# Performance work log

Hardware: AMD Instinct MI355X
Metric: run time of the kernel (lower is better)

Reference implementation:

```python
import jax, jax.numpy as jnp
import numpy as np

L, B, D, H = 2048, 2, 1024, 16
DK = D // H
SCALE = DK ** -0.5


def setup_inputs() -> dict:
    key = jax.random.key(0)
    ks = jax.random.split(key, 11)
    w_std = D ** -0.5
    return {
        "query": jax.random.normal(ks[0], (L, B, D), dtype=jnp.float32),
        "key": jax.random.normal(ks[1], (L, B, D), dtype=jnp.float32),
        "value": jax.random.normal(ks[2], (L, B, D), dtype=jnp.float32),
        "WQ_w": jax.random.normal(ks[3], (D, D), dtype=jnp.float32) * w_std,
        "WQ_b": jnp.zeros((D,), dtype=jnp.float32),
        "WK_w": jax.random.normal(ks[4], (D, D), dtype=jnp.float32) * w_std,
        "WK_b": jnp.zeros((D,), dtype=jnp.float32),
        "WV_w": jax.random.normal(ks[5], (D, D), dtype=jnp.float32) * w_std,
        "WV_b": jnp.zeros((D,), dtype=jnp.float32),
        "WO_w": jax.random.normal(ks[6], (D, D), dtype=jnp.float32) * w_std,
        "WO_b": jnp.zeros((D,), dtype=jnp.float32),
    }


def reference(query, key, value, WQ_w, WQ_b, WK_w, WK_b, WV_w, WV_b, WO_w, WO_b):
    tgt_len, batch, _ = query.shape
    src_len = key.shape[0]
    # linear projections (torch Linear: x @ W^T + b)
    q = (query @ WQ_w.T + WQ_b) * SCALE            # [L, B, D]
    k = key @ WK_w.T + WK_b                        # [S, B, D]
    v = value @ WV_w.T + WV_b                      # [S, B, D]
    # split heads: [len, B, D] -> [B*H, len, DK]
    q = q.reshape(tgt_len, batch * H, DK).transpose(1, 0, 2)
    k = k.reshape(src_len, batch * H, DK).transpose(1, 0, 2)
    v = v.reshape(src_len, batch * H, DK).transpose(1, 0, 2)
    # attention scores and softmax (full [B*H, L, S] matrix, as in the original)
    scores = jnp.einsum('nld,nsd->nls', q, k)      # [B*H, L, S]
    probs = jax.nn.softmax(scores, axis=-1)
    out = jnp.einsum('nls,nsd->nld', probs, v)     # [B*H, L, DK]
    # merge heads: [B*H, L, DK] -> [L, B, D]
    out = out.transpose(1, 0, 2).reshape(tgt_len, batch, D)
    return out @ WO_w.T + WO_b
```

## Files before the change

### kernel.cpp

```cpp
#include <hip/hip_runtime.h>
#include <hip/hip_fp16.h>

#define LL 2048
#define BB 2
#define DD 1024
#define HH 16
#define DKK 64

typedef _Float16 h8 __attribute__((ext_vector_type(8)));
typedef _Float16 h4 __attribute__((ext_vector_type(4)));
typedef float f4 __attribute__((ext_vector_type(4)));
typedef float f16v __attribute__((ext_vector_type(16)));

#define BAR() do {                                              \
    asm volatile("s_waitcnt lgkmcnt(0)" ::: "memory");          \
    __builtin_amdgcn_s_barrier();                               \
    asm volatile("" ::: "memory");                              \
} while (0)

__device__ __forceinline__ void gload_lds16(const void* g, void* l) {
    __builtin_amdgcn_global_load_lds(
        (const __attribute__((address_space(1))) void*)g,
        (__attribute__((address_space(3))) void*)l, 16, 0, 0);
}

__device__ __forceinline__ unsigned pack2h(float a, float b) {
    union { _Float16 h[2]; unsigned u; } x;
    x.h[0] = (_Float16)a; x.h[1] = (_Float16)b;
    return x.u;
}

__global__ __launch_bounds__(256) void cvt_all(
    const float* __restrict__ x0, const float* __restrict__ x1,
    const float* __restrict__ x2, const float* __restrict__ w0,
    const float* __restrict__ w1, const float* __restrict__ w2,
    const float* __restrict__ w3,
    _Float16* __restrict__ y0, _Float16* __restrict__ y1,
    _Float16* __restrict__ y2, _Float16* __restrict__ z0,
    _Float16* __restrict__ z1, _Float16* __restrict__ z2,
    _Float16* __restrict__ z3)
{
    const int sel = blockIdx.y;
    if (sel >= 3 && blockIdx.x >= 512) return;
    const float* src = (sel == 0) ? x0 : (sel == 1) ? x1 : (sel == 2) ? x2
                     : (sel == 3) ? w0 : (sel == 4) ? w1 : (sel == 5) ? w2 : w3;
    _Float16* dst = (sel == 0) ? y0 : (sel == 1) ? y1 : (sel == 2) ? y2
                  : (sel == 3) ? z0 : (sel == 4) ? z1 : (sel == 5) ? z2 : z3;
    const int i = (blockIdx.x * 256 + threadIdx.x) * 8;
    f4 a = *(const f4*)(src + i);
    f4 b = *(const f4*)(src + i + 4);
    h8 o = {(_Float16)a.x, (_Float16)a.y, (_Float16)a.z, (_Float16)a.w,
            (_Float16)b.x, (_Float16)b.y, (_Float16)b.z, (_Float16)b.w};
    *(h8*)(dst + i) = o;
}

__global__ __launch_bounds__(256) void qkv_proj(
    const _Float16* __restrict__ xq, const _Float16* __restrict__ xk,
    const _Float16* __restrict__ xv,
    const _Float16* __restrict__ wq, const float* __restrict__ bq,
    const _Float16* __restrict__ wk, const float* __restrict__ bk,
    const _Float16* __restrict__ wv, const float* __restrict__ bv,
    _Float16* __restrict__ qh, _Float16* __restrict__ kh,
    _Float16* __restrict__ vth)
{
    const int mode = blockIdx.z;
    const _Float16* X    = (mode == 0) ? xq : (mode == 1) ? xk : xv;
    const _Float16* W    = (mode == 0) ? wq : (mode == 1) ? wk : wv;
    const float*    bias = (mode == 0) ? bq : (mode == 1) ? bk : bv;

    __shared__ alignas(16) _Float16 a_sm[128 * 32];
    __shared__ alignas(16) _Float16 b_sm[128 * 32];

    const int tid  = threadIdx.x;
    const int lane = tid & 63;
    const int wave = tid >> 6;
    const int wm = (wave & 1) * 64;
    const int wn = (wave >> 1) * 64;
    const int m0 = blockIdx.x * 128;
    const int n0 = blockIdx.y * 128;

    const int srow = tid >> 2;
    const int scol = (tid & 3) * 8;
    const int lds_base = wave * 512;

    f4 acc[4][4];
    #pragma unroll
    for (int i = 0; i < 4; i++)
        #pragma unroll
        for (int j = 0; j < 4; j++)
            #pragma unroll
            for (int r = 0; r < 4; r++) acc[i][j][r] = 0.f;

    const int fr = lane & 15;
    const int fk = (lane >> 4) * 8;

    for (int k0 = 0; k0 < DD; k0 += 32) {
        gload_lds16(X + (size_t)(m0 + srow) * DD + k0 + scol,       &a_sm[lds_base]);
        gload_lds16(X + (size_t)(m0 + 64 + srow) * DD + k0 + scol,  &a_sm[2048 + lds_base]);
        gload_lds16(W + (size_t)(n0 + srow) * DD + k0 + scol,       &b_sm[lds_base]);
        gload_lds16(W + (size_t)(n0 + 64 + srow) * DD + k0 + scol,  &b_sm[2048 + lds_base]);
        __syncthreads();
        h8 af[4], bfr[4];
        #pragma unroll
        for (int i = 0; i < 4; i++) af[i]  = *(const h8*)&a_sm[(wm + i * 16 + fr) * 32 + fk];
        #pragma unroll
        for (int j = 0; j < 4; j++) bfr[j] = *(const h8*)&b_sm[(wn + j * 16 + fr) * 32 + fk];
        #pragma unroll
        for (int i = 0; i < 4; i++)
            #pragma unroll
            for (int j = 0; j < 4; j++)
                acc[i][j] = __builtin_amdgcn_mfma_f32_16x16x32_f16(af[i], bfr[j], acc[i][j], 0, 0, 0);
        __syncthreads();
    }

    const int colc = lane & 15;
    const int rowb = (lane >> 4) * 4;
    #pragma unroll
    for (int i = 0; i < 4; i++) {
        #pragma unroll
        for (int j = 0; j < 4; j++) {
            const int nn = n0 + wn + j * 16 + colc;
            const float bval = bias[nn];
            #pragma unroll
            for (int reg = 0; reg < 4; reg++) {
                const int mm = m0 + wm + i * 16 + rowb + reg;
                float v = acc[i][j][reg] + bval;
                const int b = mm & 1, l = mm >> 1;
                const int h = nn >> 6, dk = nn & 63;
                const int head = b * HH + h;
                if (mode == 0) {
                    v *= 0.1803368801111243f;
                    qh[((size_t)head * LL + l) * DKK + dk] = (_Float16)v;
                } else if (mode == 1) {
                    kh[((size_t)head * LL + l) * DKK + dk] = (_Float16)v;
                } else {
                    vth[((size_t)head * DKK + dk) * LL + l] = (_Float16)v;
                }
            }
        }
    }
}

__global__ __launch_bounds__(256, 2) void attn(
    const _Float16* __restrict__ qh, const _Float16* __restrict__ kh,
    const _Float16* __restrict__ vth, _Float16* __restrict__ oh)
{
    const int head = blockIdx.y;
    const int q0   = blockIdx.x * 128;
    const int tid = threadIdx.x, lane = tid & 63, wave = tid >> 6;
    const int qw = q0 + wave * 32;

    __shared__ alignas(16) _Float16 k_sm[128][72];
    __shared__ alignas(16) _Float16 vt_sm[64][136];
    __shared__ float ls_sm[4][32];

    const int rq = lane & 31;
    const int hi = lane >> 5;
    const int kb = hi * 8;
    const int tid8 = tid * 8;

    const _Float16* khead  = kh  + (size_t)head * LL * DKK;
    const _Float16* vthead = vth + (size_t)head * DKK * LL;

    const _Float16* qbase = qh + ((size_t)head * LL + qw + rq) * DKK;
    h8 qa[4];
    #pragma unroll
    for (int kf = 0; kf < 4; kf++) qa[kf] = *(const h8*)(qbase + kf * 16 + kb);

    f16v o0, o1;
    #pragma unroll
    for (int r = 0; r < 16; r++) { o0[r] = 0.f; o1[r] = 0.f; }
    float lsum = 0.f;

    #pragma unroll
    for (int t = 0; t < 4; t++) {
        const int flat = t * 2048 + tid8;
        *(h8*)&k_sm[flat >> 6][flat & 63] = *(const h8*)(khead + flat);
        *(h8*)&vt_sm[flat >> 7][flat & 127] =
            *(const h8*)(vthead + (size_t)(flat >> 7) * LL + (flat & 127));
    }
    BAR();

    for (int it = 0; it < 16; ++it) {
        const int s1 = it * 128 + 128;
        const bool more = (s1 < LL);

        h8 kpre[4], vpre[4];
        if (more) {
            const _Float16* kg = khead + (size_t)s1 * DKK;
            #pragma unroll
            for (int t = 0; t < 4; t++) kpre[t] = *(const h8*)(kg + t * 2048 + tid8);
            #pragma unroll
            for (int t = 0; t < 4; t++) {
                const int flat = t * 2048 + tid8;
                vpre[t] = *(const h8*)(vthead + (size_t)(flat >> 7) * LL + s1 + (flat & 127));
            }
        }

        f16v sc[4];
        #pragma unroll
        for (int st = 0; st < 4; st++) {
            #pragma unroll
            for (int r = 0; r < 16; r++) sc[st][r] = 0.f;
            #pragma unroll
            for (int kf = 0; kf < 4; kf++) {
                h8 kf8 = *(const h8*)&k_sm[st * 32 + rq][kf * 16 + kb];
                sc[st] = __builtin_amdgcn_mfma_f32_32x32x16_f16(kf8, qa[kf], sc[st], 0, 0, 0);
            }
        }

        #pragma unroll
        for (int st = 0; st < 4; st++) {
            float p[16];
            #pragma unroll
            for (int r = 0; r < 16; r++) {
                p[r] = __builtin_amdgcn_exp2f(sc[st][r]);
                lsum += p[r];
            }
            unsigned own[4][2], part[4][2];
            #pragma unroll
            for (int g = 0; g < 4; g++) {
                own[g][0] = pack2h(p[4 * g],     p[4 * g + 1]);
                own[g][1] = pack2h(p[4 * g + 2], p[4 * g + 3]);
                part[g][0] = __shfl_xor(own[g][0], 32, 64);
                part[g][1] = __shfl_xor(own[g][1], 32, 64);
            }
            #pragma unroll
            for (int j = 0; j < 2; j++) {
                union { unsigned u[4]; h8 h; } pa;
                pa.u[0] = hi ? part[2 * j + 1][0] : own[2 * j][0];
                pa.u[1] = hi ? part[2 * j + 1][1] : own[2 * j][1];
                pa.u[2] = hi ? own[2 * j + 1][0]  : part[2 * j][0];
                pa.u[3] = hi ? own[2 * j + 1][1]  : part[2 * j][1];
                h8 b0 = *(const h8*)&vt_sm[rq][st * 32 + j * 16 + kb];
                h8 b1 = *(const h8*)&vt_sm[32 + rq][st * 32 + j * 16 + kb];
                o0 = __builtin_amdgcn_mfma_f32_32x32x16_f16(pa.h, b0, o0, 0, 0, 0);
                o1 = __builtin_amdgcn_mfma_f32_32x32x16_f16(pa.h, b1, o1, 0, 0, 0);
            }
        }

        BAR();
        if (more) {
            #pragma unroll
            for (int t = 0; t < 4; t++) {
                const int flat = t * 2048 + tid8;
                *(h8*)&k_sm[flat >> 6][flat & 63] = kpre[t];
            }
            #pragma unroll
            for (int t = 0; t < 4; t++) {
                const int flat = t * 2048 + tid8;
                *(h8*)&vt_sm[flat >> 7][flat & 127] = vpre[t];
            }
            BAR();
        }
    }

    lsum += __shfl_xor(lsum, 32, 64);
    ls_sm[wave][rq] = 1.0f / lsum;
    asm volatile("s_waitcnt lgkmcnt(0)" ::: "memory");

    const int b = head >> 4, h = head & 15;
    #pragma unroll
    for (int r = 0; r < 16; r++) {
        const int qrow = (r & 3) + 8 * (r >> 2) + 4 * hi;
        const float inv = ls_sm[wave][qrow];
        const int ql = qw + qrow;
        const size_t base = (size_t)(ql * BB + b) * DD + h * DKK;
        oh[base + rq]      = (_Float16)(o0[r] * inv);
        oh[base + 32 + rq] = (_Float16)(o1[r] * inv);
    }
}

__global__ __launch_bounds__(256) void out_proj(
    const _Float16* __restrict__ oh, const _Float16* __restrict__ wo,
    const float* __restrict__ bo, float* __restrict__ out)
{
    __shared__ alignas(16) _Float16 a_sm[64 * 32];
    __shared__ alignas(16) _Float16 b_sm[128 * 32];
    const int tid = threadIdx.x, lane = tid & 63, wave = tid >> 6;
    const int wm = (wave & 1) * 32, wn = (wave >> 1) * 64;
    const int m0 = blockIdx.x * 64, n0 = blockIdx.y * 128;

    const int srow = tid >> 2;
    const int scol = (tid & 3) * 8;
    const int lds_base = wave * 512;

    f4 acc[2][4];
    #pragma unroll
    for (int i = 0; i < 2; i++)
        #pragma unroll
        for (int j = 0; j < 4; j++)
            #pragma unroll
            for (int r = 0; r < 4; r++) acc[i][j][r] = 0.f;

    const int fr = lane & 15;
    const int fk = (lane >> 4) * 8;

    for (int k0 = 0; k0 < DD; k0 += 32) {
        gload_lds16(oh + (size_t)(m0 + srow) * DD + k0 + scol,      &a_sm[lds_base]);
        gload_lds16(wo + (size_t)(n0 + srow) * DD + k0 + scol,      &b_sm[lds_base]);
        gload_lds16(wo + (size_t)(n0 + 64 + srow) * DD + k0 + scol, &b_sm[2048 + lds_base]);
        __syncthreads();
        h8 af[2], bfr[4];
        #pragma unroll
        for (int i = 0; i < 2; i++) af[i]  = *(const h8*)&a_sm[(wm + i * 16 + fr) * 32 + fk];
        #pragma unroll
        for (int j = 0; j < 4; j++) bfr[j] = *(const h8*)&b_sm[(wn + j * 16 + fr) * 32 + fk];
        #pragma unroll
        for (int i = 0; i < 2; i++)
            #pragma unroll
            for (int j = 0; j < 4; j++)
                acc[i][j] = __builtin_amdgcn_mfma_f32_16x16x32_f16(af[i], bfr[j], acc[i][j], 0, 0, 0);
        __syncthreads();
    }

    const int colc = lane & 15;
    const int rowb = (lane >> 4) * 4;
    #pragma unroll
    for (int i = 0; i < 2; i++) {
        #pragma unroll
        for (int j = 0; j < 4; j++) {
            const int nn = n0 + wn + j * 16 + colc;
            const float bval = bo[nn];
            #pragma unroll
            for (int reg = 0; reg < 4; reg++) {
                const int mm = m0 + wm + i * 16 + rowb + reg;
                out[(size_t)mm * DD + nn] = acc[i][j][reg] + bval;
            }
        }
    }
}

extern "C" void kernel_launch(void* const* d_in, const int* in_sizes, int n_in,
                              void* d_out, int out_size, void* d_ws, size_t ws_size,
                              hipStream_t stream) {
    const float* qin = (const float*)d_in[0];
    const float* kin = (const float*)d_in[1];
    const float* vin = (const float*)d_in[2];
    const float* wq  = (const float*)d_in[3];
    const float* bq  = (const float*)d_in[4];
    const float* wk  = (const float*)d_in[5];
    const float* bk  = (const float*)d_in[6];
    const float* wv  = (const float*)d_in[7];
    const float* bv  = (const float*)d_in[8];
    const float* wo  = (const float*)d_in[9];
    const float* bo  = (const float*)d_in[10];

    const size_t seg = (size_t)32 * LL * DKK;
    _Float16* qh  = (_Float16*)d_ws;
    _Float16* kh  = qh + seg;
    _Float16* vth = kh + seg;
    _Float16* oh  = vth + seg;
    _Float16* wqh = oh + seg;
    _Float16* wkh = wqh + (size_t)DD * DD;
    _Float16* wvh = wkh + (size_t)DD * DD;
    _Float16* woh = wvh + (size_t)DD * DD;
    _Float16* xqh = woh + (size_t)DD * DD;
    _Float16* xkh = xqh + seg;
    _Float16* xvh = xkh + seg;

    hipLaunchKernelGGL(cvt_all, dim3(2048, 7), dim3(256), 0, stream,
                       qin, kin, vin, wq, wk, wv, wo,
                       xqh, xkh, xvh, wqh, wkh, wvh, woh);
    hipLaunchKernelGGL(qkv_proj, dim3(32, 8, 3), dim3(256), 0, stream,
                       xqh, xkh, xvh, wqh, bq, wkh, bk, wvh, bv, qh, kh, vth);
    hipLaunchKernelGGL(attn, dim3(16, 32), dim3(256), 0, stream, qh, kh, vth, oh);
    hipLaunchKernelGGL(out_proj, dim3(64, 8), dim3(256), 0, stream, oh, woh,
                       bo, (float*)d_out);
}
```

Before: 225.7 us.

## Split key tiles across paired waves in attention and remap block order

The attention kernel now runs 512 threads per block. Two waves share each 32-row query strip, and each takes half of every 128-key tile. At the end, the partial outputs and row sums are combined through LDS, reusing the K/V tile region as the exchange buffer. Block indices are also remapped so that consecutive blocks are spread across heads and query tiles. The goal is more waves in flight per CU to hide MFMA and load latency, and better L2 locality. The costs are an extra LDS reduction and tighter register limits from __launch_bounds__(512,4), which could cause spills.

New measurement: 225.9 us. About the same (+0.1%).

```diff
diff --git a/kernel.cpp b/kernel.cpp
--- a/kernel.cpp
+++ b/kernel.cpp
@@ -141,18 +141,25 @@
     }
 }
 
-__global__ __launch_bounds__(256, 2) void attn(
+__global__ __launch_bounds__(512, 4) void attn(
     const _Float16* __restrict__ qh, const _Float16* __restrict__ kh,
     const _Float16* __restrict__ vth, _Float16* __restrict__ oh)
 {
-    const int head = blockIdx.y;
-    const int q0   = blockIdx.x * 128;
+    const int rb = blockIdx.y * 16 + blockIdx.x;
+    const int lb = (rb & 7) * 64 + (rb >> 3);
+    const int head = lb >> 4;
+    const int q0   = (lb & 15) * 128;
+
     const int tid = threadIdx.x, lane = tid & 63, wave = tid >> 6;
-    const int qw = q0 + wave * 32;
-
-    __shared__ alignas(16) _Float16 k_sm[128][72];
-    __shared__ alignas(16) _Float16 vt_sm[64][136];
-    __shared__ float ls_sm[4][32];
+    const int qstrip = wave & 3;
+    const int sh     = wave >> 2;
+    const int qw = q0 + qstrip * 32;
+
+    __shared__ alignas(16) char smem_raw[128 * 72 * 2 + 64 * 136 * 2 + 4 * 32 * 4];
+    _Float16 (*k_sm)[72]   = (_Float16(*)[72])smem_raw;
+    _Float16 (*vt_sm)[136] = (_Float16(*)[136])(smem_raw + 18432);
+    float    (*ls_sm)[32]  = (float(*)[32])(smem_raw + 18432 + 17408);
+    float*   xch           = (float*)smem_raw;
 
     const int rq = lane & 31;
     const int hi = lane >> 5;
@@ -173,8 +180,8 @@
     float lsum = 0.f;
 
     #pragma unroll
-    for (int t = 0; t < 4; t++) {
-        const int flat = t * 2048 + tid8;
+    for (int t = 0; t < 2; t++) {
+        const int flat = t * 4096 + tid8;
         *(h8*)&k_sm[flat >> 6][flat & 63] = *(const h8*)(khead + flat);
         *(h8*)&vt_sm[flat >> 7][flat & 127] =
             *(const h8*)(vthead + (size_t)(flat >> 7) * LL + (flat & 127));
@@ -185,36 +192,38 @@
         const int s1 = it * 128 + 128;
         const bool more = (s1 < LL);
 
-        h8 kpre[4], vpre[4];
+        h8 kpre[2], vpre[2];
         if (more) {
             const _Float16* kg = khead + (size_t)s1 * DKK;
             #pragma unroll
-            for (int t = 0; t < 4; t++) kpre[t] = *(const h8*)(kg + t * 2048 + tid8);
-            #pragma unroll
-            for (int t = 0; t < 4; t++) {
-                const int flat = t * 2048 + tid8;
+            for (int t = 0; t < 2; t++) kpre[t] = *(const h8*)(kg + t * 4096 + tid8);
+            #pragma unroll
+            for (int t = 0; t < 2; t++) {
+                const int flat = t * 4096 + tid8;
                 vpre[t] = *(const h8*)(vthead + (size_t)(flat >> 7) * LL + s1 + (flat & 127));
             }
         }
 
-        f16v sc[4];
-        #pragma unroll
-        for (int st = 0; st < 4; st++) {
-            #pragma unroll
-            for (int r = 0; r < 16; r++) sc[st][r] = 0.f;
+        f16v sc[2];
+        #pragma unroll
+        for (int st2 = 0; st2 < 2; st2++) {
+            const int st = sh * 2 + st2;
+            #pragma unroll
+            for (int r = 0; r < 16; r++) sc[st2][r] = 0.f;
             #pragma unroll
             for (int kf = 0; kf < 4; kf++) {
                 h8 kf8 = *(const h8*)&k_sm[st * 32 + rq][kf * 16 + kb];
-                sc[st] = __builtin_amdgcn_mfma_f32_32x32x16_f16(kf8, qa[kf], sc[st], 0, 0, 0);
-            }
-        }
-
-        #pragma unroll
-        for (int st = 0; st < 4; st++) {
+                sc[st2] = __builtin_amdgcn_mfma_f32_32x32x16_f16(kf8, qa[kf], sc[st2], 0, 0, 0);
+            }
+        }
+
+        #pragma unroll
+        for (int st2 = 0; st2 < 2; st2++) {
+            const int st = sh * 2 + st2;
             float p[16];
             #pragma unroll
             for (int r = 0; r < 16; r++) {
-                p[r] = __builtin_amdgcn_exp2f(sc[st][r]);
+                p[r] = __builtin_amdgcn_exp2f(sc[st2][r]);
                 lsum += p[r];
             }
             unsigned own[4][2], part[4][2];
@@ -242,13 +251,13 @@
         BAR();
         if (more) {
             #pragma unroll
-            for (int t = 0; t < 4; t++) {
-                const int flat = t * 2048 + tid8;
+            for (int t = 0; t < 2; t++) {
+                const int flat = t * 4096 + tid8;
                 *(h8*)&k_sm[flat >> 6][flat & 63] = kpre[t];
             }
             #pragma unroll
-            for (int t = 0; t < 4; t++) {
-                const int flat = t * 2048 + tid8;
+            for (int t = 0; t < 2; t++) {
+                const int flat = t * 4096 + tid8;
                 *(h8*)&vt_sm[flat >> 7][flat & 127] = vpre[t];
             }
             BAR();
@@ -256,18 +265,31 @@
     }
 
     lsum += __shfl_xor(lsum, 32, 64);
-    ls_sm[wave][rq] = 1.0f / lsum;
-    asm volatile("s_waitcnt lgkmcnt(0)" ::: "memory");
-
-    const int b = head >> 4, h = head & 15;
-    #pragma unroll
-    for (int r = 0; r < 16; r++) {
-        const int qrow = (r & 3) + 8 * (r >> 2) + 4 * hi;
-        const float inv = ls_sm[wave][qrow];
-        const int ql = qw + qrow;
-        const size_t base = (size_t)(ql * BB + b) * DD + h * DKK;
-        oh[base + rq]      = (_Float16)(o0[r] * inv);
-        oh[base + 32 + rq] = (_Float16)(o1[r] * inv);
+
+    float* myx = xch + ((qstrip * 64 + lane) * 33);
+    if (sh) {
+        #pragma unroll
+        for (int r = 0; r < 16; r++) { myx[r] = o0[r]; myx[16 + r] = o1[r]; }
+        myx[32] = lsum;
+    }
+    BAR();
+    if (!sh) {
+        #pragma unroll
+        for (int r = 0; r < 16; r++) { o0[r] += myx[r]; o1[r] += myx[16 + r]; }
+        lsum += myx[32];
+        ls_sm[wave][rq] = 1.0f / lsum;
+        asm volatile("s_waitcnt lgkmcnt(0)" ::: "memory");
+
+        const int b = head >> 4, h = head & 15;
+        #pragma unroll
+        for (int r = 0; r < 16; r++) {
+            const int qrow = (r & 3) + 8 * (r >> 2) + 4 * hi;
+            const float inv = ls_sm[wave][qrow];
+            const int ql = qw + qrow;
+            const size_t base = (size_t)(ql * BB + b) * DD + h * DKK;
+            oh[base + rq]      = (_Float16)(o0[r] * inv);
+            oh[base + 32 + rq] = (_Float16)(o1[r] * inv);
+        }
     }
 }
 
@@ -364,7 +386,7 @@
                        xqh, xkh, xvh, wqh, wkh, wvh, woh);
     hipLaunchKernelGGL(qkv_proj, dim3(32, 8, 3), dim3(256), 0, stream,
                        xqh, xkh, xvh, wqh, bq, wkh, bk, wvh, bv, qh, kh, vth);
-    hipLaunchKernelGGL(attn, dim3(16, 32), dim3(256), 0, stream, qh, kh, vth, oh);
+    hipLaunchKernelGGL(attn, dim3(16, 32), dim3(512), 0, stream, qh, kh, vth, oh);
     hipLaunchKernelGGL(out_proj, dim3(64, 8), dim3(256), 0, stream, oh, woh,
                        bo, (float*)d_out);
 }
```
